# Kernel optimization log

Measured on AMD Instinct MI355X. Metric: run time of the kernel, lower is better.

The kernel has to match this reference:

```python
import jax, jax.numpy as jnp
import numpy as np

N = 50000   # nodes
E = 800000  # edges per layer
D = 128     # feature dim
H = 256     # mlp hidden
O = 3       # output dim


def setup_inputs() -> dict:
    key = jax.random.key(0)
    ks = jax.random.split(key, 16)
    def lin(k, fan_out, fan_in):
        s = 1.0 / np.sqrt(fan_in)
        kw, kb = jax.random.split(k)
        return (jax.random.uniform(kw, (fan_out, fan_in), jnp.float32, -s, s),
                jax.random.uniform(kb, (fan_out,), jnp.float32, -s, s))
    x = jax.random.normal(ks[0], (N, D), jnp.float32)
    edge_idx0 = jax.random.randint(ks[1], (2, E), 0, N, dtype=jnp.int64)
    edge_idx1 = jax.random.randint(ks[2], (2, E), 0, N, dtype=jnp.int64)
    Wl1, bl1 = lin(ks[3], D, D)   # SAGE layer1: lin_l (aggregated neighbors, with bias)
    Wr1, _ = lin(ks[4], D, D)     # SAGE layer1: lin_r (root, no bias)
    Wl2, bl2 = lin(ks[5], D, D)
    Wr2, _ = lin(ks[6], D, D)
    Ws, bs = lin(ks[7], D, D)     # skip_fc
    W1, b1 = lin(ks[8], H, D)     # mlp hidden
    W2, b2 = lin(ks[9], O, H)     # mlp out
    return dict(x=x, edge_idx0=edge_idx0, edge_idx1=edge_idx1,
                Wl1=Wl1, bl1=bl1, Wr1=Wr1, Wl2=Wl2, bl2=bl2, Wr2=Wr2,
                Ws=Ws, bs=bs, W1=W1, b1=b1, W2=W2, b2=b2)


def _sage(x, ei, Wl, bl, Wr):
    # PyG SAGEConv with mean aggregation: out = lin_l(mean_j x_j) + lin_r(x_i)
    src, dst = ei[0], ei[1]
    agg = jax.ops.segment_sum(x[src], dst, num_segments=N)          # [N, D] gather-scatter
    cnt = jax.ops.segment_sum(jnp.ones((ei.shape[1],), x.dtype), dst, num_segments=N)
    agg = agg / jnp.maximum(cnt, 1.0)[:, None]
    return agg @ Wl.T + bl + x @ Wr.T


def reference(x, edge_idx0, edge_idx1, Wl1, bl1, Wr1, Wl2, bl2, Wr2,
              Ws, bs, W1, b1, W2, b2):
    inp = x
    h = _sage(x, edge_idx0, Wl1, bl1, Wr1)
    h = _sage(h, edge_idx1, Wl2, bl2, Wr2)
    h = h + (inp @ Ws.T + bs)            # skip connection
    h = jax.nn.relu(h @ W1.T + b1)       # MLP head
    return h @ W2.T + b2                  # [N, 3]
```

## Files before the change

### kernel.cpp

```cpp
#include <hip/hip_runtime.h>
#include <hip/hip_bf16.h>


#define DD 128
#define SB 8
#define CH 4096
typedef unsigned short u16;
typedef __attribute__((ext_vector_type(8))) short short8;
typedef __attribute__((ext_vector_type(4))) float f32x4;

__device__ inline u16 f2bf(float f) {
    __hip_bfloat16 h = __float2bfloat16(f);
    u16 u;
    __builtin_memcpy(&u, &h, 2);
    return u;
}
__device__ inline float bf_lo(unsigned u) { union { unsigned x; float f; } c; c.x = u << 16; return c.f; }
__device__ inline float bf_hi(unsigned u) { union { unsigned x; float f; } c; c.x = u & 0xffff0000u; return c.f; }

struct CastJobs {
    const float4* src[7];
    uint2* dst[7];
    int qstart[8];
};
__global__ __launch_bounds__(256) void cast_kernel(CastJobs jb) {
    int q = blockIdx.x * 256 + threadIdx.x;
    if (q >= jb.qstart[7]) return;
    int i = 0;
#pragma unroll
    for (int k = 1; k < 7; ++k) if (q >= jb.qstart[k]) i = k;
    int local = q - jb.qstart[i];
    float4 v = jb.src[i][local];
    unsigned lo = (unsigned)f2bf(v.x) | ((unsigned)f2bf(v.y) << 16);
    unsigned hi = (unsigned)f2bf(v.z) | ((unsigned)f2bf(v.w) << 16);
    jb.dst[i][local] = make_uint2(lo, hi);
}

__global__ __launch_bounds__(256) void hist1_kernel(const int* __restrict__ dst0, int* __restrict__ h0,
                                                    const int* __restrict__ dst1, int* __restrict__ h1,
                                                    int e0, int e1, int nb, int P) {
    int arr = blockIdx.y;
    const int* dst = arr ? dst1 : dst0;
    int* hist = arr ? h1 : h0;
    int e = arr ? e1 : e0;
    __shared__ int h[256];
    int t = threadIdx.x;
    h[t] = 0;
    __syncthreads();
    int base = blockIdx.x * CH;
    int hi = min(base + CH, e);
    for (int i = base + t; i < hi; i += 256) atomicAdd(&h[dst[i] >> SB], 1);
    __syncthreads();
    if (t < nb) hist[t * P + blockIdx.x] = h[t];
}

__global__ __launch_bounds__(256) void bscan_kernel(const int* __restrict__ h0, int* __restrict__ bb0, int* __restrict__ rp0, int e0,
                                                    const int* __restrict__ h1, int* __restrict__ bb1, int* __restrict__ rp1, int e1,
                                                    int nb, int P, int n) {
    int arr = blockIdx.x;
    const int* hist = arr ? h1 : h0;
    int* bb = arr ? bb1 : bb0;
    int* rp = arr ? rp1 : rp0;
    int E = arr ? e1 : e0;
    __shared__ int s[256];
    int t = threadIdx.x;
    int v = 0;
    if (t < nb) {
        const int* row = hist + (size_t)t * P;
        for (int p = 0; p < P; ++p) v += row[p];
    }
    s[t] = v;
    __syncthreads();
    for (int off = 1; off < 256; off <<= 1) {
        int u = (t >= off) ? s[t - off] : 0;
        __syncthreads();
        s[t] += u;
        __syncthreads();
    }
    if (t < nb) bb[t] = s[t] - v;
    if (t == 0) { bb[nb] = E; rp[n] = E; }
}

__global__ __launch_bounds__(256) void offs_kernel(int* __restrict__ h0, const int* __restrict__ bb0,
                                                   int* __restrict__ h1, const int* __restrict__ bb1,
                                                   int P) {
    int arr = blockIdx.y;
    int* hist = arr ? h1 : h0;
    const int* bb = arr ? bb1 : bb0;
    int b = blockIdx.x;
    __shared__ int s[256];
    int t = threadIdx.x;
    int v = (t < P) ? hist[b * P + t] : 0;
    s[t] = v;
    __syncthreads();
    for (int off = 1; off < 256; off <<= 1) {
        int u = (t >= off) ? s[t - off] : 0;
        __syncthreads();
        s[t] += u;
        __syncthreads();
    }
    if (t < P) hist[b * P + t] = s[t] - v + bb[b];
}

__global__ __launch_bounds__(256) void scatter1_kernel(
    const int* __restrict__ src0, const int* __restrict__ dst0, const int* __restrict__ h0, unsigned* __restrict__ binned0,
    const int* __restrict__ src1, const int* __restrict__ dst1, const int* __restrict__ h1, unsigned* __restrict__ binned1,
    int e0, int e1, int nb, int P) {
    int arr = blockIdx.y;
    const int* src = arr ? src1 : src0;
    const int* dst = arr ? dst1 : dst0;
    const int* hist = arr ? h1 : h0;
    unsigned* binned = arr ? binned1 : binned0;
    int e = arr ? e1 : e0;
    int p = blockIdx.x;
    __shared__ int cnt[256];
    int t = threadIdx.x;
    if (t < nb) cnt[t] = hist[t * P + p];
    __syncthreads();
    int base = p * CH;
    int hi = min(base + CH, e);
    for (int i = base + t; i < hi; i += 256) {
        int d = dst[i];
        int pos = atomicAdd(&cnt[d >> SB], 1);
        binned[pos] = ((unsigned)d << 16) | (unsigned)src[i];
    }
}

__global__ __launch_bounds__(256) void place_kernel(
    const unsigned* __restrict__ binned0, const int* __restrict__ bb0, int* __restrict__ rp0, u16* __restrict__ csr0,
    const unsigned* __restrict__ binned1, const int* __restrict__ bb1, int* __restrict__ rp1, u16* __restrict__ csr1,
    int n, int nb) {
    int arr = blockIdx.y;
    const unsigned* binned = arr ? binned1 : binned0;
    const int* bb = arr ? bb1 : bb0;
    int* rp = arr ? rp1 : rp0;
    u16* csr = arr ? csr1 : csr0;
    int b = blockIdx.x;
    __shared__ int cnt[256];
    __shared__ int s[256];
    int t = threadIdx.x;
    int base = bb[b], end = bb[b + 1];
    cnt[t] = 0;
    __syncthreads();
    for (int i = base + t; i < end; i += 256)
        atomicAdd(&cnt[(binned[i] >> 16) & 255], 1);
    __syncthreads();
    int deg = cnt[t];
    s[t] = deg;
    __syncthreads();
    for (int off = 1; off < 256; off <<= 1) {
        int u = (t >= off) ? s[t - off] : 0;
        __syncthreads();
        s[t] += u;
        __syncthreads();
    }
    int gpos = base + s[t] - deg;
    int node = (b << SB) + t;
    if (node < n) rp[node] = gpos;
    cnt[t] = gpos;
    __syncthreads();
    for (int i = base + t; i < end; i += 256) {
        unsigned pk = binned[i];
        int ld = (pk >> 16) & 255;
        int pos = atomicAdd(&cnt[ld], 1);
        csr[pos] = (u16)(pk & 0xffffu);
    }
}

__global__ __launch_bounds__(256) void agg_mean_bf16(const u16* __restrict__ X,
                                                     const u16* __restrict__ csr,
                                                     const int* __restrict__ rp,
                                                     u16* __restrict__ out, int n) {
    int g = (blockIdx.x * 256 + threadIdx.x) >> 4;
    int lane = threadIdx.x & 15;
    if (g >= n) return;
    int start = rp[g];
    int end = rp[g + 1];
    int d = end - start;
    const uint4* X4 = (const uint4*)X;
    float acc[8] = {0.f, 0.f, 0.f, 0.f, 0.f, 0.f, 0.f, 0.f};
    int e = start;
    for (; e + 1 < end; e += 2) {
        int s0 = csr[e], s1 = csr[e + 1];
        uint4 v0 = X4[(size_t)s0 * 16 + lane];
        uint4 v1 = X4[(size_t)s1 * 16 + lane];
        acc[0] += bf_lo(v0.x) + bf_lo(v1.x); acc[1] += bf_hi(v0.x) + bf_hi(v1.x);
        acc[2] += bf_lo(v0.y) + bf_lo(v1.y); acc[3] += bf_hi(v0.y) + bf_hi(v1.y);
        acc[4] += bf_lo(v0.z) + bf_lo(v1.z); acc[5] += bf_hi(v0.z) + bf_hi(v1.z);
        acc[6] += bf_lo(v0.w) + bf_lo(v1.w); acc[7] += bf_hi(v0.w) + bf_hi(v1.w);
    }
    if (e < end) {
        int s0 = csr[e];
        uint4 v0 = X4[(size_t)s0 * 16 + lane];
        acc[0] += bf_lo(v0.x); acc[1] += bf_hi(v0.x);
        acc[2] += bf_lo(v0.y); acc[3] += bf_hi(v0.y);
        acc[4] += bf_lo(v0.z); acc[5] += bf_hi(v0.z);
        acc[6] += bf_lo(v0.w); acc[7] += bf_hi(v0.w);
    }
    float scale = 1.0f / (float)max(d, 1);
    uint4 r;
    r.x = (unsigned)f2bf(acc[0] * scale) | ((unsigned)f2bf(acc[1] * scale) << 16);
    r.y = (unsigned)f2bf(acc[2] * scale) | ((unsigned)f2bf(acc[3] * scale) << 16);
    r.z = (unsigned)f2bf(acc[4] * scale) | ((unsigned)f2bf(acc[5] * scale) << 16);
    r.w = (unsigned)f2bf(acc[6] * scale) | ((unsigned)f2bf(acc[7] * scale) << 16);
    ((uint4*)out)[(size_t)g * 16 + lane] = r;
}

template <bool RELU>
__global__ __launch_bounds__(256) void mfma_gemm(
    const u16* __restrict__ A0, const u16* __restrict__ W0,
    const u16* __restrict__ A1, const u16* __restrict__ W1,
    const u16* __restrict__ A2, const u16* __restrict__ W2,
    int npair,
    const float* __restrict__ bias0, const float* __restrict__ bias1,
    u16* __restrict__ C, int M, int NC, int mB) {
    __shared__ u16 As[64 * 136];
    __shared__ u16 Bs[128 * 136];
    const int t = threadIdx.x;
    const int rowBase = (blockIdx.x % mB) * 64;
    const int colBase = (blockIdx.x / mB) * 128;
    const int w = t >> 6, lane = t & 63, r = lane & 15, half = lane >> 4;

    const u16* Ap[3] = {A0, A1, A2};
    const u16* Wp[3] = {W0, W1, W2};

    f32x4 acc[8];
#pragma unroll
    for (int i = 0; i < 8; ++i) acc[i] = (f32x4){0.f, 0.f, 0.f, 0.f};

    for (int p = 0; p < npair; ++p) {
        if (p) __syncthreads();
        const uint4* Ag = (const uint4*)Ap[p];
        const uint4* Wg = (const uint4*)Wp[p];
#pragma unroll
        for (int i = 0; i < 4; ++i) {
            int id = t + 256 * i, row = id >> 4, cc = id & 15;
            int gr = rowBase + row;
            uint4 v = make_uint4(0u, 0u, 0u, 0u);
            if (gr < M) v = Ag[(size_t)gr * 16 + cc];
            *(uint4*)&As[row * 136 + cc * 8] = v;
        }
#pragma unroll
        for (int i = 0; i < 8; ++i) {
            int id = t + 256 * i, row = id >> 4, cc = id & 15;
            *(uint4*)&Bs[row * 136 + cc * 8] = Wg[(size_t)(colBase + row) * 16 + cc];
        }
        __syncthreads();
        const u16* aB = &As[(w * 16 + r) * 136 + half * 8];
        const u16* bB = &Bs[r * 136 + half * 8];
#pragma unroll
        for (int kk = 0; kk < 4; ++kk) {
            short8 af = *(const short8*)(aB + kk * 32);
#pragma unroll
            for (int ct = 0; ct < 8; ++ct) {
                short8 bf = *(const short8*)(bB + ct * (16 * 136) + kk * 32);
                acc[ct] = __builtin_amdgcn_mfma_f32_16x16x32_bf16(af, bf, acc[ct], 0, 0, 0);
            }
        }
    }

#pragma unroll
    for (int ct = 0; ct < 8; ++ct) {
        int col = colBase + ct * 16 + r;
        float bv = bias0[col];
        if (bias1) bv += bias1[col];
#pragma unroll
        for (int reg = 0; reg < 4; ++reg) {
            int row = rowBase + w * 16 + half * 4 + reg;
            if (row < M) {
                float v = acc[ct][reg] + bv;
                if (RELU) v = fmaxf(v, 0.f);
                C[(size_t)row * NC + col] = f2bf(v);
            }
        }
    }
}

__global__ __launch_bounds__(256) void out_kernel(const u16* __restrict__ h4,
                                                  const float* __restrict__ W2,
                                                  const float* __restrict__ b2,
                                                  float* __restrict__ out, int n) {
    int w = (blockIdx.x * 256 + threadIdx.x) >> 6;
    int lane = threadIdx.x & 63;
    if (w >= n) return;
    uint2 hv = ((const uint2*)h4)[(size_t)w * 64 + lane];
    float h0 = bf_lo(hv.x), h1 = bf_hi(hv.x), h2 = bf_lo(hv.y), h3 = bf_hi(hv.y);
    float4 w0 = ((const float4*)W2)[0 * 64 + lane];
    float4 w1 = ((const float4*)W2)[1 * 64 + lane];
    float4 w2 = ((const float4*)W2)[2 * 64 + lane];
    float p0 = h0 * w0.x + h1 * w0.y + h2 * w0.z + h3 * w0.w;
    float p1 = h0 * w1.x + h1 * w1.y + h2 * w1.z + h3 * w1.w;
    float p2 = h0 * w2.x + h1 * w2.y + h2 * w2.z + h3 * w2.w;
#pragma unroll
    for (int off = 32; off > 0; off >>= 1) {
        p0 += __shfl_xor(p0, off);
        p1 += __shfl_xor(p1, off);
        p2 += __shfl_xor(p2, off);
    }
    if (lane == 0) {
        out[(size_t)w * 3 + 0] = p0 + b2[0];
        out[(size_t)w * 3 + 1] = p1 + b2[1];
        out[(size_t)w * 3 + 2] = p2 + b2[2];
    }
}

extern "C" void kernel_launch(void* const* d_in, const int* in_sizes, int n_in,
                              void* d_out, int out_size, void* d_ws, size_t ws_size,
                              hipStream_t stream) {
    const float* x   = (const float*)d_in[0];
    const int*   ei0 = (const int*)d_in[1];
    const int*   ei1 = (const int*)d_in[2];
    const float* Wl1 = (const float*)d_in[3];
    const float* bl1 = (const float*)d_in[4];
    const float* Wr1 = (const float*)d_in[5];
    const float* Wl2 = (const float*)d_in[6];
    const float* bl2 = (const float*)d_in[7];
    const float* Wr2 = (const float*)d_in[8];
    const float* Wsk = (const float*)d_in[9];
    const float* bsk = (const float*)d_in[10];
    const float* W1  = (const float*)d_in[11];
    const float* b1  = (const float*)d_in[12];
    const float* W2  = (const float*)d_in[13];
    const float* b2  = (const float*)d_in[14];
    float* out = (float*)d_out;

    const int N  = in_sizes[0] / DD;
    const int E0 = in_sizes[1] / 2;
    const int E1 = in_sizes[2] / 2;
    const int H  = in_sizes[12];

    const int* src0 = ei0;      const int* dst0 = ei0 + E0;
    const int* src1 = ei1;      const int* dst1 = ei1 + E1;

    const int nb   = (N + 255) >> SB;
    const int Emax = (E0 > E1) ? E0 : E1;
    const int P    = (Emax + CH - 1) / CH;

    char* wp = (char*)d_ws;
    auto carve = [&](size_t bytes) { char* p = wp; wp += (bytes + 255) & ~(size_t)255; return p; };
    u16* xh   = (u16*)carve((size_t)N * DD * 2);
    u16* aggh = (u16*)carve((size_t)N * DD * 2);
    u16* h1h  = (u16*)carve((size_t)N * DD * 2);
    u16* h3h  = (u16*)carve((size_t)N * DD * 2);
    u16* h4h  = (u16*)carve((size_t)N * H * 2);
    u16* wl1h = (u16*)carve((size_t)DD * DD * 2);
    u16* wr1h = (u16*)carve((size_t)DD * DD * 2);
    u16* wl2h = (u16*)carve((size_t)DD * DD * 2);
    u16* wr2h = (u16*)carve((size_t)DD * DD * 2);
    u16* wsh  = (u16*)carve((size_t)DD * DD * 2);
    u16* w1h  = (u16*)carve((size_t)H * DD * 2);
    int* rp0  = (int*)carve((size_t)(N + 1) * 4);
    int* rp1  = (int*)carve((size_t)(N + 1) * 4);
    u16* csr0 = (u16*)carve((size_t)E0 * 2);
    u16* csr1 = (u16*)carve((size_t)E1 * 2);
    unsigned* binned0 = (unsigned*)carve((size_t)E0 * 4);
    unsigned* binned1 = (unsigned*)carve((size_t)E1 * 4);
    int* hist1_0 = (int*)carve((size_t)nb * P * 4);
    int* hist1_1 = (int*)carve((size_t)nb * P * 4);
    int* bb0 = (int*)carve((size_t)(nb + 1) * 4);
    int* bb1 = (int*)carve((size_t)(nb + 1) * 4);

    CastJobs jb;
    const float* srcs[7] = {x, Wl1, Wr1, Wl2, Wr2, Wsk, W1};
    u16* dsts[7]         = {xh, wl1h, wr1h, wl2h, wr2h, wsh, w1h};
    int  cnts[7] = {N * DD, DD * DD, DD * DD, DD * DD, DD * DD, DD * DD, H * DD};
    int q = 0;
    for (int i = 0; i < 7; ++i) {
        jb.src[i] = (const float4*)srcs[i];
        jb.dst[i] = (uint2*)dsts[i];
        jb.qstart[i] = q;
        q += cnts[i] / 4;
    }
    jb.qstart[7] = q;

    const int gAgg = (N * 16 + 255) / 256;
    const int mB   = (N + 63) / 64;

    cast_kernel<<<(q + 255) / 256, 256, 0, stream>>>(jb);
    hist1_kernel<<<dim3(P, 2), 256, 0, stream>>>(dst0, hist1_0, dst1, hist1_1, E0, E1, nb, P);
    bscan_kernel<<<2, 256, 0, stream>>>(hist1_0, bb0, rp0, E0, hist1_1, bb1, rp1, E1, nb, P, N);
    offs_kernel<<<dim3(nb, 2), 256, 0, stream>>>(hist1_0, bb0, hist1_1, bb1, P);
    scatter1_kernel<<<dim3(P, 2), 256, 0, stream>>>(src0, dst0, hist1_0, binned0,
                                                    src1, dst1, hist1_1, binned1, E0, E1, nb, P);
    place_kernel<<<dim3(nb, 2), 256, 0, stream>>>(binned0, bb0, rp0, csr0,
                                                  binned1, bb1, rp1, csr1, N, nb);

    agg_mean_bf16<<<gAgg, 256, 0, stream>>>(xh, csr0, rp0, aggh, N);
    mfma_gemm<false><<<mB, 256, 0, stream>>>(
        aggh, wl1h, xh, wr1h, nullptr, nullptr, 2, bl1, nullptr, h1h, N, DD, mB);

    agg_mean_bf16<<<gAgg, 256, 0, stream>>>(h1h, csr1, rp1, aggh, N);
    mfma_gemm<false><<<mB, 256, 0, stream>>>(
        aggh, wl2h, h1h, wr2h, xh, wsh, 3, bl2, bsk, h3h, N, DD, mB);

    mfma_gemm<true><<<mB * (H / 128), 256, 0, stream>>>(
        h3h, w1h, nullptr, nullptr, nullptr, nullptr, 1, b1, nullptr, h4h, N, H, mB);

    const int gOut = (N * 64 + 255) / 256;
    out_kernel<<<gOut, 256, 0, stream>>>(h4h, W2, b2, out, N);
}
```

Before: 309.7 us.

## Transform-then-aggregate SAGE layers and fuse MLP head with output projection

Reorders each SAGE layer to apply the linear maps first (x@[Wl;Wr;Ws] into a concatenated buffer) and then gather-average the projected features, folding the root term, biases and skip into the aggregation epilogue. The first GEMM now reads fp32 x directly and converts it in-kernel, which removes the separate cast of x. The hidden MLP GEMM is fused with the 256->3 output projection, so the N x 256 intermediate is never written out. The trade-off is that the gathers now read from wider strided rows (384/256 columns) and that rounding happens in a different place.

```diff
diff --git a/kernel.cpp b/kernel.cpp
--- a/kernel.cpp
+++ b/kernel.cpp
@@ -15,25 +15,26 @@
     __builtin_memcpy(&u, &h, 2);
     return u;
 }
+__device__ inline unsigned pack2(float lo, float hi) {
+    return (unsigned)f2bf(lo) | ((unsigned)f2bf(hi) << 16);
+}
 __device__ inline float bf_lo(unsigned u) { union { unsigned x; float f; } c; c.x = u << 16; return c.f; }
 __device__ inline float bf_hi(unsigned u) { union { unsigned x; float f; } c; c.x = u & 0xffff0000u; return c.f; }
 
 struct CastJobs {
-    const float4* src[7];
-    uint2* dst[7];
-    int qstart[8];
+    const float4* src[6];
+    uint2* dst[6];
+    int qstart[7];
 };
 __global__ __launch_bounds__(256) void cast_kernel(CastJobs jb) {
     int q = blockIdx.x * 256 + threadIdx.x;
-    if (q >= jb.qstart[7]) return;
+    if (q >= jb.qstart[6]) return;
     int i = 0;
 #pragma unroll
-    for (int k = 1; k < 7; ++k) if (q >= jb.qstart[k]) i = k;
+    for (int k = 1; k < 6; ++k) if (q >= jb.qstart[k]) i = k;
     int local = q - jb.qstart[i];
     float4 v = jb.src[i][local];
-    unsigned lo = (unsigned)f2bf(v.x) | ((unsigned)f2bf(v.y) << 16);
-    unsigned hi = (unsigned)f2bf(v.z) | ((unsigned)f2bf(v.w) << 16);
-    jb.dst[i][local] = make_uint2(lo, hi);
+    jb.dst[i][local] = make_uint2(pack2(v.x, v.y), pack2(v.z, v.w));
 }
 
 __global__ __launch_bounds__(256) void hist1_kernel(const int* __restrict__ dst0, int* __restrict__ h0,
@@ -167,23 +168,23 @@
     }
 }
 
-__global__ __launch_bounds__(256) void agg_mean_bf16(const u16* __restrict__ X,
-                                                     const u16* __restrict__ csr,
-                                                     const int* __restrict__ rp,
-                                                     u16* __restrict__ out, int n) {
+__global__ __launch_bounds__(256) void agg1_kernel(const u16* __restrict__ G1,
+                                                   const u16* __restrict__ csr,
+                                                   const int* __restrict__ rp,
+                                                   const float* __restrict__ bl1,
+                                                   u16* __restrict__ h1, int n) {
     int g = (blockIdx.x * 256 + threadIdx.x) >> 4;
     int lane = threadIdx.x & 15;
     if (g >= n) return;
-    int start = rp[g];
-    int end = rp[g + 1];
+    int start = rp[g], end = rp[g + 1];
     int d = end - start;
-    const uint4* X4 = (const uint4*)X;
+    const uint4* X4 = (const uint4*)G1;
     float acc[8] = {0.f, 0.f, 0.f, 0.f, 0.f, 0.f, 0.f, 0.f};
     int e = start;
     for (; e + 1 < end; e += 2) {
         int s0 = csr[e], s1 = csr[e + 1];
-        uint4 v0 = X4[(size_t)s0 * 16 + lane];
-        uint4 v1 = X4[(size_t)s1 * 16 + lane];
+        uint4 v0 = X4[(size_t)s0 * 48 + lane];
+        uint4 v1 = X4[(size_t)s1 * 48 + lane];
         acc[0] += bf_lo(v0.x) + bf_lo(v1.x); acc[1] += bf_hi(v0.x) + bf_hi(v1.x);
         acc[2] += bf_lo(v0.y) + bf_lo(v1.y); acc[3] += bf_hi(v0.y) + bf_hi(v1.y);
         acc[4] += bf_lo(v0.z) + bf_lo(v1.z); acc[5] += bf_hi(v0.z) + bf_hi(v1.z);
@@ -191,29 +192,80 @@
     }
     if (e < end) {
         int s0 = csr[e];
-        uint4 v0 = X4[(size_t)s0 * 16 + lane];
+        uint4 v0 = X4[(size_t)s0 * 48 + lane];
         acc[0] += bf_lo(v0.x); acc[1] += bf_hi(v0.x);
         acc[2] += bf_lo(v0.y); acc[3] += bf_hi(v0.y);
         acc[4] += bf_lo(v0.z); acc[5] += bf_hi(v0.z);
         acc[6] += bf_lo(v0.w); acc[7] += bf_hi(v0.w);
     }
-    float scale = 1.0f / (float)max(d, 1);
+    float sc = 1.0f / (float)max(d, 1);
+    uint4 m = X4[(size_t)g * 48 + 16 + lane];
+    const float4* bl = (const float4*)bl1;
+    float4 ba = bl[lane * 2], bb = bl[lane * 2 + 1];
     uint4 r;
-    r.x = (unsigned)f2bf(acc[0] * scale) | ((unsigned)f2bf(acc[1] * scale) << 16);
-    r.y = (unsigned)f2bf(acc[2] * scale) | ((unsigned)f2bf(acc[3] * scale) << 16);
-    r.z = (unsigned)f2bf(acc[4] * scale) | ((unsigned)f2bf(acc[5] * scale) << 16);
-    r.w = (unsigned)f2bf(acc[6] * scale) | ((unsigned)f2bf(acc[7] * scale) << 16);
-    ((uint4*)out)[(size_t)g * 16 + lane] = r;
-}
-
-template <bool RELU>
-__global__ __launch_bounds__(256) void mfma_gemm(
-    const u16* __restrict__ A0, const u16* __restrict__ W0,
-    const u16* __restrict__ A1, const u16* __restrict__ W1,
-    const u16* __restrict__ A2, const u16* __restrict__ W2,
-    int npair,
-    const float* __restrict__ bias0, const float* __restrict__ bias1,
-    u16* __restrict__ C, int M, int NC, int mB) {
+    r.x = pack2(acc[0] * sc + bf_lo(m.x) + ba.x, acc[1] * sc + bf_hi(m.x) + ba.y);
+    r.y = pack2(acc[2] * sc + bf_lo(m.y) + ba.z, acc[3] * sc + bf_hi(m.y) + ba.w);
+    r.z = pack2(acc[4] * sc + bf_lo(m.z) + bb.x, acc[5] * sc + bf_hi(m.z) + bb.y);
+    r.w = pack2(acc[6] * sc + bf_lo(m.w) + bb.z, acc[7] * sc + bf_hi(m.w) + bb.w);
+    ((uint4*)h1)[(size_t)g * 16 + lane] = r;
+}
+
+__global__ __launch_bounds__(256) void agg2_kernel(const u16* __restrict__ G2,
+                                                   const u16* __restrict__ G1,
+                                                   const u16* __restrict__ csr,
+                                                   const int* __restrict__ rp,
+                                                   const float* __restrict__ bl2,
+                                                   const float* __restrict__ bs,
+                                                   u16* __restrict__ h3, int n) {
+    int g = (blockIdx.x * 256 + threadIdx.x) >> 4;
+    int lane = threadIdx.x & 15;
+    if (g >= n) return;
+    int start = rp[g], end = rp[g + 1];
+    int d = end - start;
+    const uint4* X4 = (const uint4*)G2;
+    float acc[8] = {0.f, 0.f, 0.f, 0.f, 0.f, 0.f, 0.f, 0.f};
+    int e = start;
+    for (; e + 1 < end; e += 2) {
+        int s0 = csr[e], s1 = csr[e + 1];
+        uint4 v0 = X4[(size_t)s0 * 32 + lane];
+        uint4 v1 = X4[(size_t)s1 * 32 + lane];
+        acc[0] += bf_lo(v0.x) + bf_lo(v1.x); acc[1] += bf_hi(v0.x) + bf_hi(v1.x);
+        acc[2] += bf_lo(v0.y) + bf_lo(v1.y); acc[3] += bf_hi(v0.y) + bf_hi(v1.y);
+        acc[4] += bf_lo(v0.z) + bf_lo(v1.z); acc[5] += bf_hi(v0.z) + bf_hi(v1.z);
+        acc[6] += bf_lo(v0.w) + bf_lo(v1.w); acc[7] += bf_hi(v0.w) + bf_hi(v1.w);
+    }
+    if (e < end) {
+        int s0 = csr[e];
+        uint4 v0 = X4[(size_t)s0 * 32 + lane];
+        acc[0] += bf_lo(v0.x); acc[1] += bf_hi(v0.x);
+        acc[2] += bf_lo(v0.y); acc[3] += bf_hi(v0.y);
+        acc[4] += bf_lo(v0.z); acc[5] += bf_hi(v0.z);
+        acc[6] += bf_lo(v0.w); acc[7] += bf_hi(v0.w);
+    }
+    float sc = 1.0f / (float)max(d, 1);
+    uint4 m2 = X4[(size_t)g * 32 + 16 + lane];
+    uint4 m1 = ((const uint4*)G1)[(size_t)g * 48 + 32 + lane];
+    const float4* c2 = (const float4*)bl2;
+    const float4* cs = (const float4*)bs;
+    float4 ba = c2[lane * 2], bb = c2[lane * 2 + 1];
+    float4 sa = cs[lane * 2], sb = cs[lane * 2 + 1];
+    uint4 r;
+    r.x = pack2(acc[0] * sc + bf_lo(m2.x) + bf_lo(m1.x) + ba.x + sa.x,
+                acc[1] * sc + bf_hi(m2.x) + bf_hi(m1.x) + ba.y + sa.y);
+    r.y = pack2(acc[2] * sc + bf_lo(m2.y) + bf_lo(m1.y) + ba.z + sa.z,
+                acc[3] * sc + bf_hi(m2.y) + bf_hi(m1.y) + ba.w + sa.w);
+    r.z = pack2(acc[4] * sc + bf_lo(m2.z) + bf_lo(m1.z) + bb.x + sb.x,
+                acc[5] * sc + bf_hi(m2.z) + bf_hi(m1.z) + bb.y + sb.y);
+    r.w = pack2(acc[6] * sc + bf_lo(m2.w) + bf_lo(m1.w) + bb.z + sb.z,
+                acc[7] * sc + bf_hi(m2.w) + bf_hi(m1.w) + bb.w + sb.w);
+    ((uint4*)h3)[(size_t)g * 16 + lane] = r;
+}
+
+template <bool F32A>
+__global__ __launch_bounds__(256) void mfma_gemm(const void* __restrict__ Av,
+                                                 const u16* __restrict__ W,
+                                                 const float* __restrict__ bias,
+                                                 u16* __restrict__ C, int M, int NC, int mB) {
     __shared__ u16 As[64 * 136];
     __shared__ u16 Bs[128 * 136];
     const int t = threadIdx.x;
@@ -221,29 +273,96 @@
     const int colBase = (blockIdx.x / mB) * 128;
     const int w = t >> 6, lane = t & 63, r = lane & 15, half = lane >> 4;
 
-    const u16* Ap[3] = {A0, A1, A2};
-    const u16* Wp[3] = {W0, W1, W2};
-
     f32x4 acc[8];
 #pragma unroll
     for (int i = 0; i < 8; ++i) acc[i] = (f32x4){0.f, 0.f, 0.f, 0.f};
 
-    for (int p = 0; p < npair; ++p) {
-        if (p) __syncthreads();
-        const uint4* Ag = (const uint4*)Ap[p];
-        const uint4* Wg = (const uint4*)Wp[p];
-#pragma unroll
-        for (int i = 0; i < 4; ++i) {
-            int id = t + 256 * i, row = id >> 4, cc = id & 15;
-            int gr = rowBase + row;
-            uint4 v = make_uint4(0u, 0u, 0u, 0u);
-            if (gr < M) v = Ag[(size_t)gr * 16 + cc];
-            *(uint4*)&As[row * 136 + cc * 8] = v;
+#pragma unroll
+    for (int i = 0; i < 4; ++i) {
+        int id = t + 256 * i, row = id >> 4, cc = id & 15;
+        int gr = rowBase + row;
+        uint4 v = make_uint4(0u, 0u, 0u, 0u);
+        if (gr < M) {
+            if (F32A) {
+                const float* A = (const float*)Av;
+                float4 a = *(const float4*)&A[(size_t)gr * DD + cc * 8];
+                float4 b = *(const float4*)&A[(size_t)gr * DD + cc * 8 + 4];
+                v = make_uint4(pack2(a.x, a.y), pack2(a.z, a.w), pack2(b.x, b.y), pack2(b.z, b.w));
+            } else {
+                v = ((const uint4*)Av)[(size_t)gr * 16 + cc];
+            }
+        }
+        *(uint4*)&As[row * 136 + cc * 8] = v;
+    }
+#pragma unroll
+    for (int i = 0; i < 8; ++i) {
+        int id = t + 256 * i, row = id >> 4, cc = id & 15;
+        *(uint4*)&Bs[row * 136 + cc * 8] = ((const uint4*)W)[(size_t)(colBase + row) * 16 + cc];
+    }
+    __syncthreads();
+    const u16* aB = &As[(w * 16 + r) * 136 + half * 8];
+    const u16* bB = &Bs[r * 136 + half * 8];
+#pragma unroll
+    for (int kk = 0; kk < 4; ++kk) {
+        short8 af = *(const short8*)(aB + kk * 32);
+#pragma unroll
+        for (int ct = 0; ct < 8; ++ct) {
+            short8 bf = *(const short8*)(bB + ct * (16 * 136) + kk * 32);
+            acc[ct] = __builtin_amdgcn_mfma_f32_16x16x32_bf16(af, bf, acc[ct], 0, 0, 0);
+        }
+    }
+
+#pragma unroll
+    for (int ct = 0; ct < 8; ++ct) {
+        int col = colBase + ct * 16 + r;
+        float bv = bias ? bias[col] : 0.f;
+#pragma unroll
+        for (int reg = 0; reg < 4; ++reg) {
+            int row = rowBase + w * 16 + half * 4 + reg;
+            if (row < M) C[(size_t)row * NC + col] = f2bf(acc[ct][reg] + bv);
+        }
+    }
+}
+
+__global__ __launch_bounds__(256) void gemm_out_kernel(const u16* __restrict__ h3,
+                                                       const u16* __restrict__ W1,
+                                                       const float* __restrict__ b1,
+                                                       const float* __restrict__ W2,
+                                                       const float* __restrict__ b2,
+                                                       float* __restrict__ out, int M) {
+    __shared__ u16 As[64 * 136];
+    __shared__ u16 Bs[128 * 136];
+    __shared__ float w2s[3 * 256];
+    __shared__ float b1s[256];
+    const int t = threadIdx.x;
+    const int rowBase = blockIdx.x * 64;
+    const int w = t >> 6, lane = t & 63, r = lane & 15, half = lane >> 4;
+
+    for (int i = t; i < 768; i += 256) w2s[i] = W2[i];
+    b1s[t] = b1[t];
+#pragma unroll
+    for (int i = 0; i < 4; ++i) {
+        int id = t + 256 * i, row = id >> 4, cc = id & 15;
+        int gr = rowBase + row;
+        uint4 v = make_uint4(0u, 0u, 0u, 0u);
+        if (gr < M) v = ((const uint4*)h3)[(size_t)gr * 16 + cc];
+        *(uint4*)&As[row * 136 + cc * 8] = v;
+    }
+
+    f32x4 acc[2][8];
+#pragma unroll
+    for (int ch = 0; ch < 2; ++ch)
+#pragma unroll
+        for (int i = 0; i < 8; ++i) acc[ch][i] = (f32x4){0.f, 0.f, 0.f, 0.f};
+
+    for (int ch = 0; ch < 2; ++ch) {
+        __syncthreads();
+        if (ch) {
         }
 #pragma unroll
         for (int i = 0; i < 8; ++i) {
             int id = t + 256 * i, row = id >> 4, cc = id & 15;
-            *(uint4*)&Bs[row * 136 + cc * 8] = Wg[(size_t)(colBase + row) * 16 + cc];
+            *(uint4*)&Bs[row * 136 + cc * 8] = ((const uint4*)W1)[(size_t)(ch * 128 + row) * 16 + cc];
         }
         __syncthreads();
         const u16* aB = &As[(w * 16 + r) * 136 + half * 8];
@@ -254,53 +373,44 @@
 #pragma unroll
             for (int ct = 0; ct < 8; ++ct) {
                 short8 bf = *(const short8*)(bB + ct * (16 * 136) + kk * 32);
-                acc[ct] = __builtin_amdgcn_mfma_f32_16x16x32_bf16(af, bf, acc[ct], 0, 0, 0);
+                acc[ch][ct] = __builtin_amdgcn_mfma_f32_16x16x32_bf16(af, bf, acc[ch][ct], 0, 0, 0);
             }
         }
     }
 
-#pragma unroll
-    for (int ct = 0; ct < 8; ++ct) {
-        int col = colBase + ct * 16 + r;
-        float bv = bias0[col];
-        if (bias1) bv += bias1[col];
+    float p[4][3] = {{0.f}};
+#pragma unroll
+    for (int ch = 0; ch < 2; ++ch) {
+#pragma unroll
+        for (int ct = 0; ct < 8; ++ct) {
+            int col = ch * 128 + ct * 16 + r;
+            float bv = b1s[col];
+            float w0 = w2s[0 * 256 + col], w1 = w2s[1 * 256 + col], w2v = w2s[2 * 256 + col];
+#pragma unroll
+            for (int reg = 0; reg < 4; ++reg) {
+                float h4 = fmaxf(acc[ch][ct][reg] + bv, 0.f);
+                p[reg][0] += h4 * w0;
+                p[reg][1] += h4 * w1;
+                p[reg][2] += h4 * w2v;
+            }
+        }
+    }
+#pragma unroll
+    for (int m = 1; m < 16; m <<= 1)
+#pragma unroll
+        for (int reg = 0; reg < 4; ++reg)
+#pragma unroll
+            for (int o = 0; o < 3; ++o) p[reg][o] += __shfl_xor(p[reg][o], m);
+    if (r == 0) {
 #pragma unroll
         for (int reg = 0; reg < 4; ++reg) {
             int row = rowBase + w * 16 + half * 4 + reg;
             if (row < M) {
-                float v = acc[ct][reg] + bv;
-                if (RELU) v = fmaxf(v, 0.f);
-                C[(size_t)row * NC + col] = f2bf(v);
+                out[(size_t)row * 3 + 0] = p[reg][0] + b2[0];
+                out[(size_t)row * 3 + 1] = p[reg][1] + b2[1];
+                out[(size_t)row * 3 + 2] = p[reg][2] + b2[2];
             }
         }
-    }
-}
-
-__global__ __launch_bounds__(256) void out_kernel(const u16* __restrict__ h4,
-                                                  const float* __restrict__ W2,
-                                                  const float* __restrict__ b2,
-                                                  float* __restrict__ out, int n) {
-    int w = (blockIdx.x * 256 + threadIdx.x) >> 6;
-    int lane = threadIdx.x & 63;
-    if (w >= n) return;
-    uint2 hv = ((const uint2*)h4)[(size_t)w * 64 + lane];
-    float h0 = bf_lo(hv.x), h1 = bf_hi(hv.x), h2 = bf_lo(hv.y), h3 = bf_hi(hv.y);
-    float4 w0 = ((const float4*)W2)[0 * 64 + lane];
-    float4 w1 = ((const float4*)W2)[1 * 64 + lane];
-    float4 w2 = ((const float4*)W2)[2 * 64 + lane];
-    float p0 = h0 * w0.x + h1 * w0.y + h2 * w0.z + h3 * w0.w;
-    float p1 = h0 * w1.x + h1 * w1.y + h2 * w1.z + h3 * w1.w;
-    float p2 = h0 * w2.x + h1 * w2.y + h2 * w2.z + h3 * w2.w;
-#pragma unroll
-    for (int off = 32; off > 0; off >>= 1) {
-        p0 += __shfl_xor(p0, off);
-        p1 += __shfl_xor(p1, off);
-        p2 += __shfl_xor(p2, off);
-    }
-    if (lane == 0) {
-        out[(size_t)w * 3 + 0] = p0 + b2[0];
-        out[(size_t)w * 3 + 1] = p1 + b2[1];
-        out[(size_t)w * 3 + 2] = p2 + b2[2];
     }
 }
 
@@ -338,16 +448,12 @@
 
     char* wp = (char*)d_ws;
     auto carve = [&](size_t bytes) { char* p = wp; wp += (bytes + 255) & ~(size_t)255; return p; };
-    u16* xh   = (u16*)carve((size_t)N * DD * 2);
-    u16* aggh = (u16*)carve((size_t)N * DD * 2);
+    u16* G1   = (u16*)carve((size_t)N * 384 * 2);
+    u16* G2   = (u16*)carve((size_t)N * 256 * 2);
     u16* h1h  = (u16*)carve((size_t)N * DD * 2);
     u16* h3h  = (u16*)carve((size_t)N * DD * 2);
-    u16* h4h  = (u16*)carve((size_t)N * H * 2);
-    u16* wl1h = (u16*)carve((size_t)DD * DD * 2);
-    u16* wr1h = (u16*)carve((size_t)DD * DD * 2);
-    u16* wl2h = (u16*)carve((size_t)DD * DD * 2);
-    u16* wr2h = (u16*)carve((size_t)DD * DD * 2);
-    u16* wsh  = (u16*)carve((size_t)DD * DD * 2);
+    u16* wc1  = (u16*)carve((size_t)384 * DD * 2);
+    u16* wc2  = (u16*)carve((size_t)256 * DD * 2);
     u16* w1h  = (u16*)carve((size_t)H * DD * 2);
     int* rp0  = (int*)carve((size_t)(N + 1) * 4);
     int* rp1  = (int*)carve((size_t)(N + 1) * 4);
@@ -361,17 +467,17 @@
     int* bb1 = (int*)carve((size_t)(nb + 1) * 4);
 
     CastJobs jb;
-    const float* srcs[7] = {x, Wl1, Wr1, Wl2, Wr2, Wsk, W1};
-    u16* dsts[7]         = {xh, wl1h, wr1h, wl2h, wr2h, wsh, w1h};
-    int  cnts[7] = {N * DD, DD * DD, DD * DD, DD * DD, DD * DD, DD * DD, H * DD};
+    const float* srcs[6] = {Wl1, Wr1, Wsk, Wl2, Wr2, W1};
+    u16* dsts[6] = {wc1, wc1 + 128 * DD, wc1 + 256 * DD, wc2, wc2 + 128 * DD, w1h};
+    int  cnts[6] = {DD * DD, DD * DD, DD * DD, DD * DD, DD * DD, H * DD};
     int q = 0;
-    for (int i = 0; i < 7; ++i) {
+    for (int i = 0; i < 6; ++i) {
         jb.src[i] = (const float4*)srcs[i];
         jb.dst[i] = (uint2*)dsts[i];
         jb.qstart[i] = q;
         q += cnts[i] / 4;
     }
-    jb.qstart[7] = q;
+    jb.qstart[6] = q;
 
     const int gAgg = (N * 16 + 255) / 256;
     const int mB   = (N + 63) / 64;
@@ -385,17 +491,9 @@
     place_kernel<<<dim3(nb, 2), 256, 0, stream>>>(binned0, bb0, rp0, csr0,
                                                   binned1, bb1, rp1, csr1, N, nb);
 
-    agg_mean_bf16<<<gAgg, 256, 0, stream>>>(xh, csr0, rp0, aggh, N);
-    mfma_gemm<false><<<mB, 256, 0, stream>>>(
-        aggh, wl1h, xh, wr1h, nullptr, nullptr, 2, bl1, nullptr, h1h, N, DD, mB);
-
-    agg_mean_bf16<<<gAgg, 256, 0, stream>>>(h1h, csr1, rp1, aggh, N);
-    mfma_gemm<false><<<mB, 256, 0, stream>>>(
-        aggh, wl2h, h1h, wr2h, xh, wsh, 3, bl2, bsk, h3h, N, DD, mB);
-
-    mfma_gemm<true><<<mB * (H / 128), 256, 0, stream>>>(
-        h3h, w1h, nullptr, nullptr, nullptr, nullptr, 1, b1, nullptr, h4h, N, H, mB);
-
-    const int gOut = (N * 64 + 255) / 256;
-    out_kernel<<<gOut, 256, 0, stream>>>(h4h, W2, b2, out, N);
-}
+    mfma_gemm<true><<<mB * 3, 256, 0, stream>>>(x, wc1, nullptr, G1, N, 384, mB);
+    agg1_kernel<<<gAgg, 256, 0, stream>>>(G1, csr0, rp0, bl1, h1h, N);
+    mfma_gemm<false><<<mB * 2, 256, 0, stream>>>(h1h, wc2, nullptr, G2, N, 256, mB);
+    agg2_kernel<<<gAgg, 256, 0, stream>>>(G2, G1, csr1, rp1, bl2, bsk, h3h, N);
+    gemm_out_kernel<<<mB, 256, 0, stream>>>(h3h, w1h, b1, W2, b2, out, N);
+}
```

Measured after the change: 294.2 us. 1.05x faster.
